# Performance work log

Hardware: AMD Instinct MI355X
Metric: run time of the kernel (lower is better)

## Reference

```python
import jax, jax.numpy as jnp
import numpy as np

THRESH = 0.7
MIN_KEPT = 100000


def setup_inputs() -> dict:
    key = jax.random.key(0)
    k1, k2 = jax.random.split(key)
    N, C, H, W = 4, 19, 512, 1024
    logits = jax.random.normal(k1, (N, C, H, W), dtype=jnp.float32)
    targets = jax.random.randint(k2, (N, H, W), 0, C, dtype=jnp.int64)
    return {"logits": logits, "targets": targets}


def reference(logits, targets):
    # log_softmax over class dim, then per-pixel NLL gather.  [N,C,H,W] -> [N,H,W]
    log_p = jax.nn.log_softmax(logits, axis=1)
    nll = -jnp.take_along_axis(log_p, targets[:, None, :, :], axis=1)[:, 0]
    loss_flat = nll.reshape(-1)

    valid = loss_flat > 0  # mirrors `loss_flat > 0` validity test in torch code
    n_valid = valid.sum()

    # Descending sort with invalid pixels pushed to the end (-inf).
    sorted_loss = jnp.sort(jnp.where(valid, loss_flat, -jnp.inf))[::-1]

    n_keep = jnp.maximum(jnp.int32(MIN_KEPT), (THRESH * n_valid).astype(jnp.int32))
    n_keep = jnp.minimum(n_keep, n_valid.astype(jnp.int32))
    thresh_val = sorted_loss[jnp.maximum(n_keep - 1, 0)]

    mask = loss_flat >= thresh_val
    kept_sum = jnp.sum(jnp.where(mask, loss_flat, jnp.float32(0)))
    kept_cnt = jnp.maximum(mask.sum(), 1).astype(loss_flat.dtype)
    ohem_mean = kept_sum / kept_cnt

    # If no valid pixels, torch returns loss_flat.mean()
    return jnp.where(n_valid > 0, ohem_mean, loss_flat.mean())
```

## Files before the change

kernel.cpp:

```cpp
#include <hip/hip_runtime.h>

#define NBATCH 4
#define NCLS   19
#define HW     524288
#define NPIX   (NBATCH * HW)
#define NQ     (NPIX / 4)

#define NCOPY   8
#define NBINS   2048
#define H0        0
#define H1        (NCOPY * NBINS)
#define CT_BASE   (2 * NCOPY * NBINS)
#define CT_SUM    CT_BASE
#define CT_CNT    (CT_BASE + 2)
#define CT_TICKET (CT_BASE + 3)
#define CT_BAR    (CT_BASE + 4)
#define CTRL_U32  (CT_BASE + 8)
#define LOSS_OFF  262144

#define LH_BLOCKS 512
#define FU_BLOCKS 512

__global__ __launch_bounds__(256) void loss_hist_k(const float* __restrict__ logits,
                                                   const int* __restrict__ targets,
                                                   float* __restrict__ loss,
                                                   unsigned* __restrict__ hist0) {
    __shared__ unsigned sh[NBINS];
    for (int i = threadIdx.x; i < NBINS; i += 256) sh[i] = 0u;
    __syncthreads();

    int tid = blockIdx.x * 256 + threadIdx.x;
#pragma unroll 1
    for (int q = tid; q < NQ; q += LH_BLOCKS * 256) {
        int p   = q << 2;
        int n   = p >> 19;
        int pix = p & (HW - 1);
        const float4* base = reinterpret_cast<const float4*>(
            logits + (size_t)n * NCLS * HW + pix);
        int4 t4 = *reinterpret_cast<const int4*>(targets + p);

        float s0 = 0.f, s1 = 0.f, s2 = 0.f, s3 = 0.f;
        float g0 = 0.f, g1 = 0.f, g2 = 0.f, g3 = 0.f;
#pragma unroll
        for (int c = 0; c < NCLS; ++c) {
            float4 val = base[c * (HW / 4)];
            s0 += __expf(val.x); s1 += __expf(val.y);
            s2 += __expf(val.z); s3 += __expf(val.w);
            if (c == t4.x) g0 = val.x;
            if (c == t4.y) g1 = val.y;
            if (c == t4.z) g2 = val.z;
            if (c == t4.w) g3 = val.w;
        }
        float l0 = __logf(s0) - g0;
        float l1 = __logf(s1) - g1;
        float l2 = __logf(s2) - g2;
        float l3 = __logf(s3) - g3;
        *reinterpret_cast<float4*>(loss + p) = make_float4(l0, l1, l2, l3);

        if (l0 > 0.f) atomicAdd(&sh[__float_as_uint(l0) >> 21], 1u);
        if (l1 > 0.f) atomicAdd(&sh[__float_as_uint(l1) >> 21], 1u);
        if (l2 > 0.f) atomicAdd(&sh[__float_as_uint(l2) >> 21], 1u);
        if (l3 > 0.f) atomicAdd(&sh[__float_as_uint(l3) >> 21], 1u);
    }
    __syncthreads();
    unsigned* g = hist0 + (blockIdx.x & (NCOPY - 1)) * NBINS;
    for (int i = threadIdx.x; i < NBINS; i += 256) {
        unsigned vv = sh[i];
        if (vv) atomicAdd(&g[i], vv);
    }
}

__device__ __forceinline__ void scan_hist(const unsigned* __restrict__ ghist,
                                          unsigned* sh_h, unsigned* sh_c,
                                          unsigned* bcast, unsigned k_in,
                                          bool derive_k) {
    int t = threadIdx.x;
    for (int i = t; i < NBINS; i += 256) {
        unsigned s = 0;
#pragma unroll
        for (int k = 0; k < NCOPY; ++k) s += ghist[k * NBINS + i];
        sh_h[i] = s;
    }
    __syncthreads();
    unsigned s = 0;
#pragma unroll
    for (int j = 0; j < 8; ++j) s += sh_h[t * 8 + j];
    sh_c[t] = s;
    __syncthreads();
    if (t == 0) {
        unsigned k = k_in, flag = 0;
        unsigned total = 0;
        for (int i = 0; i < 256; ++i) total += sh_c[i];
        if (derive_k) {
            if (total == 0) { flag = 1u; k = 1u; }
            else {
                long long kk = (long long)(0.7f * (float)total);
                if (kk < 100000) kk = 100000;
                if (kk > (long long)total) kk = (long long)total;
                k = (unsigned)kk;
            }
        }
        unsigned run = 0; int chunk = -1;
        for (int i = 255; i >= 0; --i) {
            if (run + sh_c[i] >= k) { chunk = i; break; }
            run += sh_c[i];
        }
        unsigned sel = 0, rank = 1;
        if (chunk >= 0) {
            for (int b = chunk * 8 + 7; b >= chunk * 8; --b) {
                if (run + sh_h[b] >= k) { sel = (unsigned)b; rank = k - run; break; }
                run += sh_h[b];
            }
        }
        bcast[0] = sel; bcast[1] = rank; bcast[2] = flag; bcast[3] = total;
    }
    __syncthreads();
}

__global__ __launch_bounds__(256, 2) void fused_k(const float4* __restrict__ loss4,
                                                  unsigned* __restrict__ ctrl,
                                                  float* __restrict__ out) {
    __shared__ unsigned h[NBINS];
    __shared__ unsigned c2[256];
    __shared__ unsigned bcast[4];

    scan_hist(ctrl + H0, h, c2, bcast, 0u, true);
    unsigned sel0 = bcast[0], rank1 = bcast[1], flag = bcast[2];
    __syncthreads();

    int tid = blockIdx.x * 256 + threadIdx.x;
    if (!flag) {
        for (int i = threadIdx.x; i < NBINS; i += 256) h[i] = 0u;
        __syncthreads();
#pragma unroll 1
        for (int q = tid; q < NQ; q += FU_BLOCKS * 256) {
            float4 v = loss4[q];
#define PROC(X) do { float x_ = (X); if (x_ > 0.f) { unsigned u_ = __float_as_uint(x_); \
            if ((u_ >> 21) == sel0) atomicAdd(&h[(u_ >> 10) & 0x7FFu], 1u); } } while (0)
            PROC(v.x); PROC(v.y); PROC(v.z); PROC(v.w);
#undef PROC
        }
        __syncthreads();
        unsigned* g = ctrl + H1 + (blockIdx.x & (NCOPY - 1)) * NBINS;
        for (int i = threadIdx.x; i < NBINS; i += 256) {
            unsigned vv = h[i];
            if (vv) atomicAdd(&g[i], vv);
        }
    }

    __syncthreads();
    if (threadIdx.x == 0) {
        __hip_atomic_fetch_add(&ctrl[CT_BAR], 1u, __ATOMIC_ACQ_REL, __HIP_MEMORY_SCOPE_AGENT);
        while (__hip_atomic_load(&ctrl[CT_BAR], __ATOMIC_ACQUIRE, __HIP_MEMORY_SCOPE_AGENT)
               < (unsigned)FU_BLOCKS) {
            __builtin_amdgcn_s_sleep(2);
        }
    }
    __syncthreads();

    float thresh;
    if (flag) {
        thresh = -__builtin_inff();
    } else {
        scan_hist(ctrl + H1, h, c2, bcast, rank1, false);
        thresh = __uint_as_float((sel0 << 21) | (bcast[0] << 10));
    }

    double lsum = 0.0; unsigned lcnt = 0;
#pragma unroll 1
    for (int q = tid; q < NQ; q += FU_BLOCKS * 256) {
        float4 v = loss4[q];
        if (v.x >= thresh) { lsum += (double)v.x; lcnt++; }
        if (v.y >= thresh) { lsum += (double)v.y; lcnt++; }
        if (v.z >= thresh) { lsum += (double)v.z; lcnt++; }
        if (v.w >= thresh) { lsum += (double)v.w; lcnt++; }
    }
    __shared__ double sd[256];
    __shared__ unsigned sc[256];
    int t = threadIdx.x;
    sd[t] = lsum; sc[t] = lcnt;
    __syncthreads();
    for (int o = 128; o > 0; o >>= 1) {
        if (t < o) { sd[t] += sd[t + o]; sc[t] += sc[t + o]; }
        __syncthreads();
    }
    if (t == 0) {
        atomicAdd(reinterpret_cast<double*>(ctrl + CT_SUM), sd[0]);
        atomicAdd(&ctrl[CT_CNT], sc[0]);
        __threadfence();
        unsigned tick = atomicAdd(&ctrl[CT_TICKET], 1u);
        if (tick == (unsigned)(FU_BLOCKS - 1)) {
            double ssum = atomicAdd(reinterpret_cast<double*>(ctrl + CT_SUM), 0.0);
            unsigned cc = atomicAdd(&ctrl[CT_CNT], 0u);
            if (cc < 1u) cc = 1u;
            out[0] = (float)(ssum / (double)cc);
        }
    }
}

extern "C" void kernel_launch(void* const* d_in, const int* in_sizes, int n_in,
                              void* d_out, int out_size, void* d_ws, size_t ws_size,
                              hipStream_t stream) {
    const float* logits  = (const float*)d_in[0];
    const int*   targets = (const int*)d_in[1];
    float* out = (float*)d_out;
    unsigned* ctrl = (unsigned*)d_ws;
    float* loss = (float*)((char*)d_ws + LOSS_OFF);
    const float4* loss4 = (const float4*)loss;

    hipMemsetAsync(ctrl, 0, CTRL_U32 * sizeof(unsigned), stream);
    loss_hist_k<<<LH_BLOCKS, 256, 0, stream>>>(logits, targets, loss, ctrl + H0);
    fused_k<<<FU_BLOCKS, 256, 0, stream>>>(loss4, ctrl, out);
}
```

Measured before the change: 125.3 us.

## Keep loss values in registers across grid barrier instead of rereading

Each thread of the fused kernel now loads its four float4 loss values once, before the second histogram pass, and keeps them in registers through the grid-wide barrier for the final thresholded sum. This removes the second full pass over the loss buffer from global memory. The spin-wait is also reworked to sleep longer and poll with an atomic add of zero, and the second histogram is read with relaxed atomic loads so it sees other blocks' writes. The change relies on NQ being exactly four times the thread count and adds register pressure.

```diff
diff --git a/kernel.cpp b/kernel.cpp
--- a/kernel.cpp
+++ b/kernel.cpp
@@ -20,6 +20,7 @@
 
 #define LH_BLOCKS 512
 #define FU_BLOCKS 512
+#define FU_THREADS (FU_BLOCKS * 256)
 
 __global__ __launch_bounds__(256) void loss_hist_k(const float* __restrict__ logits,
                                                    const int* __restrict__ targets,
@@ -73,12 +74,16 @@
 __device__ __forceinline__ void scan_hist(const unsigned* __restrict__ ghist,
                                           unsigned* sh_h, unsigned* sh_c,
                                           unsigned* bcast, unsigned k_in,
-                                          bool derive_k) {
+                                          bool derive_k, bool bypass) {
     int t = threadIdx.x;
     for (int i = t; i < NBINS; i += 256) {
         unsigned s = 0;
 #pragma unroll
-        for (int k = 0; k < NCOPY; ++k) s += ghist[k * NBINS + i];
+        for (int k = 0; k < NCOPY; ++k) {
+            s += bypass ? __hip_atomic_load(&ghist[k * NBINS + i],
+                                            __ATOMIC_RELAXED, __HIP_MEMORY_SCOPE_AGENT)
+                        : ghist[k * NBINS + i];
+        }
         sh_h[i] = s;
     }
     __syncthreads();
@@ -124,22 +129,26 @@
     __shared__ unsigned c2[256];
     __shared__ unsigned bcast[4];
 
-    scan_hist(ctrl + H0, h, c2, bcast, 0u, true);
+    scan_hist(ctrl + H0, h, c2, bcast, 0u, true, false);
     unsigned sel0 = bcast[0], rank1 = bcast[1], flag = bcast[2];
     __syncthreads();
 
     int tid = blockIdx.x * 256 + threadIdx.x;
+    float4 v0 = loss4[tid];
+    float4 v1 = loss4[tid + FU_THREADS];
+    float4 v2 = loss4[tid + 2 * FU_THREADS];
+    float4 v3 = loss4[tid + 3 * FU_THREADS];
+
+    for (int i = threadIdx.x; i < NBINS; i += 256) h[i] = 0u;
+    __syncthreads();
     if (!flag) {
-        for (int i = threadIdx.x; i < NBINS; i += 256) h[i] = 0u;
-        __syncthreads();
-#pragma unroll 1
-        for (int q = tid; q < NQ; q += FU_BLOCKS * 256) {
-            float4 v = loss4[q];
 #define PROC(X) do { float x_ = (X); if (x_ > 0.f) { unsigned u_ = __float_as_uint(x_); \
-            if ((u_ >> 21) == sel0) atomicAdd(&h[(u_ >> 10) & 0x7FFu], 1u); } } while (0)
-            PROC(v.x); PROC(v.y); PROC(v.z); PROC(v.w);
+        if ((u_ >> 21) == sel0) atomicAdd(&h[(u_ >> 10) & 0x7FFu], 1u); } } while (0)
+        PROC(v0.x); PROC(v0.y); PROC(v0.z); PROC(v0.w);
+        PROC(v1.x); PROC(v1.y); PROC(v1.z); PROC(v1.w);
+        PROC(v2.x); PROC(v2.y); PROC(v2.z); PROC(v2.w);
+        PROC(v3.x); PROC(v3.y); PROC(v3.z); PROC(v3.w);
 #undef PROC
-        }
         __syncthreads();
         unsigned* g = ctrl + H1 + (blockIdx.x & (NCOPY - 1)) * NBINS;
         for (int i = threadIdx.x; i < NBINS; i += 256) {
@@ -151,10 +160,12 @@
     __syncthreads();
     if (threadIdx.x == 0) {
         __hip_atomic_fetch_add(&ctrl[CT_BAR], 1u, __ATOMIC_ACQ_REL, __HIP_MEMORY_SCOPE_AGENT);
-        while (__hip_atomic_load(&ctrl[CT_BAR], __ATOMIC_ACQUIRE, __HIP_MEMORY_SCOPE_AGENT)
-               < (unsigned)FU_BLOCKS) {
-            __builtin_amdgcn_s_sleep(2);
-        }
+        unsigned cur;
+        do {
+            __builtin_amdgcn_s_sleep(16);
+            cur = __hip_atomic_fetch_add(&ctrl[CT_BAR], 0u,
+                                         __ATOMIC_ACQUIRE, __HIP_MEMORY_SCOPE_AGENT);
+        } while (cur < (unsigned)FU_BLOCKS);
     }
     __syncthreads();
 
@@ -162,19 +173,18 @@
     if (flag) {
         thresh = -__builtin_inff();
     } else {
-        scan_hist(ctrl + H1, h, c2, bcast, rank1, false);
+        scan_hist(ctrl + H1, h, c2, bcast, rank1, false, true);
         thresh = __uint_as_float((sel0 << 21) | (bcast[0] << 10));
     }
 
     double lsum = 0.0; unsigned lcnt = 0;
-#pragma unroll 1
-    for (int q = tid; q < NQ; q += FU_BLOCKS * 256) {
-        float4 v = loss4[q];
-        if (v.x >= thresh) { lsum += (double)v.x; lcnt++; }
-        if (v.y >= thresh) { lsum += (double)v.y; lcnt++; }
-        if (v.z >= thresh) { lsum += (double)v.z; lcnt++; }
-        if (v.w >= thresh) { lsum += (double)v.w; lcnt++; }
-    }
+#define ACC(X) do { float x_ = (X); if (x_ >= thresh) { lsum += (double)x_; lcnt++; } } while (0)
+    ACC(v0.x); ACC(v0.y); ACC(v0.z); ACC(v0.w);
+    ACC(v1.x); ACC(v1.y); ACC(v1.z); ACC(v1.w);
+    ACC(v2.x); ACC(v2.y); ACC(v2.z); ACC(v2.w);
+    ACC(v3.x); ACC(v3.y); ACC(v3.z); ACC(v3.w);
+#undef ACC
+
     __shared__ double sd[256];
     __shared__ unsigned sc[256];
     int t = threadIdx.x;
```

Result: faster. 121.4 us (median of 2 runs) (-3.1%).
